# Optimization experiments

Hardware: AMD Instinct MI355X
Metric: run time of the kernel (lower is better)

Reference implementation:

```python
import jax, jax.numpy as jnp
import numpy as np

EPS_BN = 1e-5
EPS_LN = 1e-5
EPS_L2 = 1e-12


def adder2d(x, w, stride):
    """AdderNet pseudo-conv: out = -sum |x_patch - w| (negative L1 distance).
    x: (N, Cin, H, W); w: (Cout, Cin, kh, kw); no padding, no bias.
    Loops only over the small fixed kernel footprint (<=12 positions) to avoid
    materializing the full im2col L1 tensor at once.
    """
    N, Cin, H, W = x.shape
    Cout, _, kh, kw = w.shape
    sh, sw = stride
    Ho = (H - kh) // sh + 1
    Wo = (W - kw) // sw + 1
    out = jnp.zeros((N, Ho, Wo, Cout), dtype=x.dtype)
    for i in range(kh):
        for j in range(kw):
            # strided slice of the input for this kernel tap: (N, Cin, Ho, Wo)
            xs = x[:, :, i:i + sh * Ho:sh, j:j + sw * Wo:sw]
            xs = jnp.transpose(xs, (0, 2, 3, 1))          # (N, Ho, Wo, Cin)
            wt = w[:, :, i, j]                            # (Cout, Cin)
            # |x - w| summed over Cin -> (N, Ho, Wo, Cout)
            out = out - jnp.abs(xs[:, :, :, None, :] - wt[None, None, None, :, :]).sum(-1)
    return jnp.transpose(out, (0, 3, 1, 2))               # (N, Cout, Ho, Wo)


def bn_relu(x, gamma, beta):
    # training-mode BatchNorm2d (batch statistics, biased var) + ReLU
    mean = x.mean(axis=(0, 2, 3), keepdims=True)
    var = x.var(axis=(0, 2, 3), keepdims=True)
    y = (x - mean) * jax.lax.rsqrt(var + EPS_BN)
    y = y * gamma[None, :, None, None] + beta[None, :, None, None]
    return jax.nn.relu(y)


def setup_inputs() -> dict:
    key = jax.random.key(0)
    ks = jax.random.split(key, 8)
    N = 16
    x = jax.random.normal(ks[0], (N, 1, 196, 3), dtype=jnp.float32)
    w1 = jax.random.normal(ks[1], (128, 1, 6, 1), dtype=jnp.float32) * 0.1
    w2 = jax.random.normal(ks[2], (256, 128, 6, 1), dtype=jnp.float32) * 0.05
    w3 = jax.random.normal(ks[3], (384, 256, 6, 2), dtype=jnp.float32) * 0.05
    g1, b1 = jnp.ones((128,), jnp.float32), jnp.zeros((128,), jnp.float32)
    g2, b2 = jnp.ones((256,), jnp.float32), jnp.zeros((256,), jnp.float32)
    g3, b3 = jnp.ones((384,), jnp.float32), jnp.zeros((384,), jnp.float32)
    Wfc = jax.random.normal(ks[4], (6, 16128), dtype=jnp.float32) * (1.0 / np.sqrt(16128))
    bfc = jax.random.normal(ks[5], (6,), dtype=jnp.float32) * 0.01
    return {"x": x, "w1": w1, "g1": g1, "b1": b1, "w2": w2, "g2": g2, "b2": b2,
            "w3": w3, "g3": g3, "b3": b3, "Wfc": Wfc, "bfc": bfc}


def reference(x, w1, g1, b1, w2, g2, b2, w3, g3, b3, Wfc, bfc):
    h = bn_relu(adder2d(x, w1, (2, 1)), g1, b1)   # (N,128,96,3)
    h = bn_relu(adder2d(h, w2, (2, 1)), g2, b2)   # (N,256,46,3)
    h = bn_relu(adder2d(h, w3, (2, 1)), g3, b3)   # (N,384,21,2)
    h = h.reshape(h.shape[0], -1)                  # (N,16128)
    h = h @ Wfc.T + bfc                            # (N,6)
    # nn.LayerNorm(x.size()) normalizes over ALL dims (batch included), weight=1 bias=0
    mu = h.mean()
    var = h.var()
    h = (h - mu) * jax.lax.rsqrt(var + EPS_LN)
    # F.normalize: per-row L2 normalization
    norm = jnp.sqrt((h * h).sum(axis=1, keepdims=True))
    return h / jnp.maximum(norm, EPS_L2)
```

## Files before the change

### kernel.cpp

```cpp
#include <hip/hip_runtime.h>
#include <math.h>

#define DEVINL __device__ __forceinline__

DEVINL float absadd(float a, float b) {
  float t;
  asm("v_add_f32 %0, |%1|, |%2|" : "=v"(t) : "v"(a), "v"(b));
  return t;
}

template<int NWAVES>
DEVINL void block_reduce_2d(double& a, double& b) {
  #pragma unroll
  for (int off = 32; off > 0; off >>= 1) {
    a += __shfl_down(a, off, 64);
    b += __shfl_down(b, off, 64);
  }
  __shared__ double sa[NWAVES], sb[NWAVES];
  const int tid = threadIdx.x;
  const int wid = tid >> 6;
  if ((tid & 63) == 0) { sa[wid] = a; sb[wid] = b; }
  __syncthreads();
  if (tid == 0) {
    double ta = 0.0, tb = 0.0;
    #pragma unroll
    for (int w = 0; w < NWAVES; ++w) { ta += sa[w]; tb += sb[w]; }
    a = ta; b = tb;
  }
}

__global__ __launch_bounds__(256) void k_conv1(
    const float* __restrict__ x, const float* __restrict__ w1,
    const float* __restrict__ g1, const float* __restrict__ b1,
    float* __restrict__ h1) {
  __shared__ float xlds[9408];
  const int co = blockIdx.x;
  const int tid = threadIdx.x;
  {
    float4* xd = (float4*)xlds;
    const float4* xs = (const float4*)x;
    #pragma unroll
    for (int k = 0; k < 10; ++k) {
      const int f = tid + k * 256;
      if (f < 2352) xd[f] = xs[f];
    }
  }
  float wv[6];
  #pragma unroll
  for (int i = 0; i < 6; ++i) wv[i] = w1[co * 6 + i];
  __syncthreads();

  float vals[18];
  double s = 0.0, sq = 0.0;
  #pragma unroll
  for (int k = 0; k < 18; ++k) {
    const int p = tid + k * 256;
    const int n = p / 288;
    const int r = p - n * 288;
    const int ho = r / 3;
    const int wo = r - ho * 3;
    const float* xb = xlds + n * 588 + (2 * ho) * 3 + wo;
    float e0 = xb[0]  - wv[0];
    float e1 = xb[3]  - wv[1];
    float e2 = xb[6]  - wv[2];
    float e3 = xb[9]  - wv[3];
    float e4 = xb[12] - wv[4];
    float e5 = xb[15] - wv[5];
    const float t0 = absadd(e0, e1);
    const float t1 = absadd(e2, e3);
    const float t2 = absadd(e4, e5);
    const float v = -((t0 + t1) + t2);
    vals[k] = v;
    s += (double)v;
    sq += (double)v * (double)v;
  }
  block_reduce_2d<4>(s, sq);
  __shared__ float ssc, ssh;
  if (tid == 0) {
    const double mean = s * (1.0 / 4608.0);
    const double var  = sq * (1.0 / 4608.0) - mean * mean;
    const float rstd = (float)rsqrt(var + 1e-5);
    const float sc = g1[co] * rstd;
    ssc = sc;
    ssh = b1[co] - (float)mean * sc;
  }
  __syncthreads();
  const float sc = ssc, sh = ssh;
  #pragma unroll
  for (int k = 0; k < 18; ++k) {
    const int p = tid + k * 256;
    const int n = p / 288;
    const int r = p - n * 288;
    const int ho = r / 3;
    const int wo = r - ho * 3;
    h1[((n * 128 + co) * 96 + ho) * 3 + wo] = fmaxf(0.f, fmaf(vals[k], sc, sh));
  }
}

__global__ __launch_bounds__(192) void k_conv2p(
    const float* __restrict__ h1, const float* __restrict__ w2,
    float* __restrict__ part2) {
  __shared__ float wlds[512];
  __shared__ float4 xbuf[2][584];
  const int bx = blockIdx.x;
  const int kc = bx & 7;
  const int rbx = bx >> 3;
  const int cg = rbx & 63;
  const int nh = rbx >> 6;
  const int co0 = cg * 4, ci0 = kc * 16, n0 = nh * 8;
  const int tid = threadIdx.x;
  #pragma unroll
  for (int f = tid; f < 512; f += 192) {
    const int cil = f >> 5, rem = f & 31, c = rem >> 3, kk = rem & 7;
    wlds[f] = (kk < 6) ? w2[(co0 + c) * 768 + (ci0 + cil) * 6 + kk] : 0.f;
  }
  const bool active = tid < 184;
  const int n = tid / 23, hp = tid - n * 23;

  int s_lds[3], s_g[3];
  #pragma unroll
  for (int k = 0; k < 3; ++k) {
    const int f = tid + k * 192;
    const int nn = f / 72, j = f - nn * 72;
    s_lds[k] = nn * 73 + j;
    s_g[k]   = (n0 + nn) * 9216 + j;
  }
  const float4* h1v = (const float4*)h1;

  float acc[4][6];
  #pragma unroll
  for (int c = 0; c < 4; ++c)
    #pragma unroll
    for (int o = 0; o < 6; ++o) acc[c][o] = 0.f;

  float4 r[3];
  #pragma unroll
  for (int k = 0; k < 3; ++k) r[k] = h1v[s_g[k] + ci0 * 72];
  #pragma unroll
  for (int k = 0; k < 3; ++k) xbuf[0][s_lds[k]] = r[k];
  #pragma unroll
  for (int k = 0; k < 3; ++k) r[k] = h1v[s_g[k] + (ci0 + 1) * 72];
  __syncthreads();

  const float4* wl4 = (const float4*)wlds;
  #pragma unroll 1
  for (int ci = 0; ci < 16; ++ci) {
    const float4* cur = xbuf[ci & 1];
    if (ci + 1 < 16) {
      float4* nxt = xbuf[(ci + 1) & 1];
      #pragma unroll
      for (int k = 0; k < 3; ++k) nxt[s_lds[k]] = r[k];
    }
    if (ci + 2 < 16) {
      #pragma unroll
      for (int k = 0; k < 3; ++k) r[k] = h1v[s_g[k] + (ci0 + ci + 2) * 72];
    }
    if (active) {
      const float4* xr = cur + n * 73 + hp * 3;
      float xf[24];
      #pragma unroll
      for (int t = 0; t < 6; ++t) {
        const float4 q = xr[t];
        xf[4 * t + 0] = q.x; xf[4 * t + 1] = q.y; xf[4 * t + 2] = q.z; xf[4 * t + 3] = q.w;
      }
      #pragma unroll
      for (int c = 0; c < 4; ++c) {
        const float4 wa = wl4[(ci * 4 + c) * 2];
        const float4 wb = wl4[(ci * 4 + c) * 2 + 1];
        const float wv[6] = {wa.x, wa.y, wa.z, wa.w, wb.x, wb.y};
        #pragma unroll
        for (int po = 0; po < 2; ++po)
          #pragma unroll
          for (int wo = 0; wo < 3; ++wo) {
            float e0 = xf[(2 * po + 0) * 3 + wo] - wv[0];
            float e1 = xf[(2 * po + 1) * 3 + wo] - wv[1];
            float e2 = xf[(2 * po + 2) * 3 + wo] - wv[2];
            float e3 = xf[(2 * po + 3) * 3 + wo] - wv[3];
            float e4 = xf[(2 * po + 4) * 3 + wo] - wv[4];
            float e5 = xf[(2 * po + 5) * 3 + wo] - wv[5];
            const float t0 = absadd(e0, e1);
            const float t1 = absadd(e2, e3);
            const float t2 = absadd(e4, e5);
            acc[c][po * 3 + wo] += (t0 + t1) + t2;
          }
      }
    }
    __syncthreads();
  }
  if (active) {
    #pragma unroll
    for (int c = 0; c < 4; ++c)
      #pragma unroll
      for (int po = 0; po < 2; ++po)
        #pragma unroll
        for (int wo = 0; wo < 3; ++wo) {
          const int p = (n0 + n) * 138 + (2 * hp + po) * 3 + wo;
          part2[(size_t)(kc * 256 + co0 + c) * 2208 + p] = acc[c][po * 3 + wo];
        }
  }
}

__global__ __launch_bounds__(384) void k_combine2(
    const float* __restrict__ part2, const float* __restrict__ g2,
    const float* __restrict__ b2, float* __restrict__ h2) {
  const int co = blockIdx.x;
  const int tid = threadIdx.x;
  const bool active = tid < 368;
  float v[6];
  double s = 0.0, sq = 0.0;
  #pragma unroll
  for (int k = 0; k < 6; ++k) {
    float sum = 0.f;
    if (active) {
      const int p = tid + k * 368;
      #pragma unroll
      for (int kc = 0; kc < 8; ++kc)
        sum += part2[(size_t)(kc * 256 + co) * 2208 + p];
    }
    const float val = -sum;
    v[k] = val;
    if (active) { s += (double)val; sq += (double)val * (double)val; }
  }
  block_reduce_2d<6>(s, sq);
  __shared__ float ssc, ssh;
  if (tid == 0) {
    const double mean = s * (1.0 / 2208.0);
    const double var  = sq * (1.0 / 2208.0) - mean * mean;
    const float rstd = (float)rsqrt(var + 1e-5);
    const float sc = g2[co] * rstd;
    ssc = sc;
    ssh = b2[co] - (float)mean * sc;
  }
  __syncthreads();
  if (active) {
    const float sc = ssc, sh = ssh;
    #pragma unroll
    for (int k = 0; k < 6; ++k) {
      const int p = tid + k * 368;
      const int n = p / 138, rem = p - n * 138;
      h2[n * 35328 + co * 138 + rem] = fmaxf(0.f, fmaf(v[k], sc, sh));
    }
  }
}

__global__ __launch_bounds__(128) void k_conv3p(
    const float* __restrict__ h2, const float* __restrict__ w3,
    float* __restrict__ part3) {
  __shared__ float wlds[768];
  __shared__ float2 xbuf[2][1136];
  const int bx = blockIdx.x;
  const int cg = bx >> 4, kc = bx & 15;
  const int co0 = cg * 4, ci0 = kc * 16;
  const int tid = threadIdx.x;
  #pragma unroll
  for (int f = tid; f < 768; f += 128) {
    const int cil = f / 48, rem = f - cil * 48, c = rem / 12, kk = rem - c * 12;
    wlds[f] = w3[(co0 + c) * 3072 + (ci0 + cil) * 12 + kk];
  }
  const bool active = tid < 112;
  const int n = tid / 7, hot = tid - n * 7;

  int s_lds[9], s_g[9];
  const bool v9 = tid < 80;
  #pragma unroll
  for (int k = 0; k < 9; ++k) {
    const int f = tid + k * 128;
    const int nn = f / 69, j = f - nn * 69;
    s_lds[k] = nn * 71 + j;
    s_g[k]   = nn * 17664 + j;
  }
  const float2* h2v = (const float2*)h2;

  float acc[4][3][2];
  #pragma unroll
  for (int c = 0; c < 4; ++c)
    #pragma unroll
    for (int h = 0; h < 3; ++h) { acc[c][h][0] = 0.f; acc[c][h][1] = 0.f; }

  float2 r[9];
  #pragma unroll
  for (int k = 0; k < 8; ++k) r[k] = h2v[s_g[k] + ci0 * 69];
  if (v9) r[8] = h2v[s_g[8] + ci0 * 69];
  #pragma unroll
  for (int k = 0; k < 8; ++k) xbuf[0][s_lds[k]] = r[k];
  if (v9) xbuf[0][s_lds[8]] = r[8];
  #pragma unroll
  for (int k = 0; k < 8; ++k) r[k] = h2v[s_g[k] + (ci0 + 1) * 69];
  if (v9) r[8] = h2v[s_g[8] + (ci0 + 1) * 69];
  __syncthreads();

  const float4* wl4 = (const float4*)wlds;
  #pragma unroll 1
  for (int ci = 0; ci < 16; ++ci) {
    const float2* cur = xbuf[ci & 1];
    if (ci + 1 < 16) {
      float2* nxt = xbuf[(ci + 1) & 1];
      #pragma unroll
      for (int k = 0; k < 8; ++k) nxt[s_lds[k]] = r[k];
      if (v9) nxt[s_lds[8]] = r[8];
    }
    if (ci + 2 < 16) {
      #pragma unroll
      for (int k = 0; k < 8; ++k) r[k] = h2v[s_g[k] + (ci0 + ci + 2) * 69];
      if (v9) r[8] = h2v[s_g[8] + (ci0 + ci + 2) * 69];
    }
    if (active) {
      float xf[30];
      const float2* xr = cur + n * 71 + 9 * hot;
      #pragma unroll
      for (int t = 0; t < 15; ++t) {
        const float2 q = xr[t];
        xf[2 * t + 0] = q.x; xf[2 * t + 1] = q.y;
      }
      #pragma unroll
      for (int c = 0; c < 4; ++c) {
        const float4 w0 = wl4[(ci * 4 + c) * 3];
        const float4 w1 = wl4[(ci * 4 + c) * 3 + 1];
        const float4 w2q = wl4[(ci * 4 + c) * 3 + 2];
        const float wv[12] = {w0.x, w0.y, w0.z, w0.w, w1.x, w1.y,
                              w1.z, w1.w, w2q.x, w2q.y, w2q.z, w2q.w};
        #pragma unroll
        for (int h = 0; h < 3; ++h)
          #pragma unroll
          for (int wo = 0; wo < 2; ++wo) {
            float e0  = xf[(2 * h + 0) * 3 + wo]     - wv[0];
            float e1  = xf[(2 * h + 0) * 3 + wo + 1] - wv[1];
            float e2  = xf[(2 * h + 1) * 3 + wo]     - wv[2];
            float e3  = xf[(2 * h + 1) * 3 + wo + 1] - wv[3];
            float e4  = xf[(2 * h + 2) * 3 + wo]     - wv[4];
            float e5  = xf[(2 * h + 2) * 3 + wo + 1] - wv[5];
            float e6  = xf[(2 * h + 3) * 3 + wo]     - wv[6];
            float e7  = xf[(2 * h + 3) * 3 + wo + 1] - wv[7];
            float e8  = xf[(2 * h + 4) * 3 + wo]     - wv[8];
            float e9  = xf[(2 * h + 4) * 3 + wo + 1] - wv[9];
            float e10 = xf[(2 * h + 5) * 3 + wo]     - wv[10];
            float e11 = xf[(2 * h + 5) * 3 + wo + 1] - wv[11];
            const float t0 = absadd(e0, e1);
            const float t1 = absadd(e2, e3);
            const float t2 = absadd(e4, e5);
            const float t3 = absadd(e6, e7);
            const float t4 = absadd(e8, e9);
            const float t5 = absadd(e10, e11);
            acc[c][h][wo] += ((t0 + t1) + (t2 + t3)) + (t4 + t5);
          }
      }
    }
    __syncthreads();
  }
  if (active) {
    #pragma unroll
    for (int c = 0; c < 4; ++c)
      #pragma unroll
      for (int h = 0; h < 3; ++h) {
        const int ho = 3 * hot + h;
        #pragma unroll
        for (int wo = 0; wo < 2; ++wo) {
          const int p = n * 42 + ho * 2 + wo;
          part3[(size_t)(kc * 384 + co0 + c) * 672 + p] = acc[c][h][wo];
        }
      }
  }
}

__global__ __launch_bounds__(384) void k_combine3(
    const float* __restrict__ part3, const float* __restrict__ g3,
    const float* __restrict__ b3, float* __restrict__ h3) {
  const int co = blockIdx.x;
  const int tid = threadIdx.x;
  const bool active = tid < 336;
  float v[2];
  double s = 0.0, sq = 0.0;
  #pragma unroll
  for (int k = 0; k < 2; ++k) {
    float sum = 0.f;
    if (active) {
      const int p = tid + k * 336;
      #pragma unroll
      for (int kc = 0; kc < 16; ++kc)
        sum += part3[(size_t)(kc * 384 + co) * 672 + p];
    }
    const float val = -sum;
    v[k] = val;
    if (active) { s += (double)val; sq += (double)val * (double)val; }
  }
  block_reduce_2d<6>(s, sq);
  __shared__ float ssc, ssh;
  if (tid == 0) {
    const double mean = s * (1.0 / 672.0);
    const double var  = sq * (1.0 / 672.0) - mean * mean;
    const float rstd = (float)rsqrt(var + 1e-5);
    const float sc = g3[co] * rstd;
    ssc = sc;
    ssh = b3[co] - (float)mean * sc;
  }
  __syncthreads();
  if (active) {
    const float sc = ssc, sh = ssh;
    #pragma unroll
    for (int k = 0; k < 2; ++k) {
      const int p = tid + k * 336;
      const int n = p / 42, rem = p - n * 42;
      h3[n * 16128 + co * 42 + rem] = fmaxf(0.f, fmaf(v[k], sc, sh));
    }
  }
}

__global__ __launch_bounds__(256) void k_fcp(
    const float* __restrict__ h3, const float* __restrict__ Wfc,
    float* __restrict__ hfcp) {
  const int bx = blockIdx.x;
  const int pair = bx >> 2, q = bx & 3;
  const int n = pair / 6, o = pair - n * 6;
  const float4* xr = (const float4*)(h3 + n * 16128) + q * 1008;
  const float4* wr = (const float4*)(Wfc + o * 16128) + q * 1008;
  float sacc = 0.f;
  for (int k = threadIdx.x; k < 1008; k += 256) {
    const float4 xv = xr[k];
    const float4 wv = wr[k];
    sacc += xv.x * wv.x + xv.y * wv.y + xv.z * wv.z + xv.w * wv.w;
  }
  double d = (double)sacc, dummy = 0.0;
  block_reduce_2d<4>(d, dummy);
  if (threadIdx.x == 0) hfcp[bx] = (float)d;
}

__global__ __launch_bounds__(128) void k_final(
    const float* __restrict__ hfcp, const float* __restrict__ bfc,
    float* __restrict__ out) {
  __shared__ float ys[96];
  __shared__ float params[2];
  const int tid = threadIdx.x;
  float v = 0.f;
  if (tid < 96) {
    v = hfcp[tid * 4 + 0] + hfcp[tid * 4 + 1] + hfcp[tid * 4 + 2] + hfcp[tid * 4 + 3]
        + bfc[tid % 6];
    ys[tid] = v;
  }
  __syncthreads();
  if (tid == 0) {
    double s = 0.0, sq = 0.0;
    for (int i = 0; i < 96; ++i) { const double t = (double)ys[i]; s += t; sq += t * t; }
    const double mu = s / 96.0;
    const double var = sq / 96.0 - mu * mu;
    params[0] = (float)mu;
    params[1] = (float)rsqrt(var + 1e-5);
  }
  __syncthreads();
  const float y = (v - params[0]) * params[1];
  __syncthreads();
  if (tid < 96) ys[tid] = y;
  __syncthreads();
  if (tid < 96) {
    const int n = tid / 6;
    float ss = 0.f;
    #pragma unroll
    for (int k = 0; k < 6; ++k) { const float t = ys[n * 6 + k]; ss += t * t; }
    const float norm = sqrtf(ss);
    out[tid] = y / fmaxf(norm, 1e-12f);
  }
}

extern "C" void kernel_launch(void* const* d_in, const int* in_sizes, int n_in,
                              void* d_out, int out_size, void* d_ws, size_t ws_size,
                              hipStream_t stream) {
  const float* x   = (const float*)d_in[0];
  const float* w1  = (const float*)d_in[1];
  const float* g1  = (const float*)d_in[2];
  const float* b1  = (const float*)d_in[3];
  const float* w2  = (const float*)d_in[4];
  const float* g2  = (const float*)d_in[5];
  const float* b2  = (const float*)d_in[6];
  const float* w3  = (const float*)d_in[7];
  const float* g3  = (const float*)d_in[8];
  const float* b3  = (const float*)d_in[9];
  const float* Wfc = (const float*)d_in[10];
  const float* bfc = (const float*)d_in[11];

  float* ws   = (float*)d_ws;
  float* h1   = ws;
  float* h2   = h1 + 589824;
  float* h3   = h2 + 565248;
  float* hfcp = h3 + 258048;
  float* part = hfcp + 384;
  float* out  = (float*)d_out;

  k_conv1   <<<128, 256, 0, stream>>>(x, w1, g1, b1, h1);
  k_conv2p  <<<1024, 192, 0, stream>>>(h1, w2, part);
  k_combine2<<<256, 384, 0, stream>>>(part, g2, b2, h2);
  k_conv3p  <<<1536, 128, 0, stream>>>(h2, w3, part);
  k_combine3<<<384, 384, 0, stream>>>(part, g3, b3, h3);
  k_fcp     <<<384, 256, 0, stream>>>(h3, Wfc, hfcp);
  k_final   <<<1, 128, 0, stream>>>(hfcp, bfc, out);
}
```

Measured before the change: 132.3 us.

## Remap conv3 work so each lane owns one output channel across all rows

The layer-3 adder kernel is retiled into single-wave blocks of 64 threads. Each block covers 8 output channels and 8 batch items, and each lane owns one channel and one sample, accumulating all 42 outputs in registers. The input row is slid through a register window across the 7 row groups. The double-buffered LDS and __syncthreads are replaced by a single buffer, relying on one-wave lockstep execution. Output is stored as contiguous float2. This removes block barriers and the idle lanes of the old mapping, at the cost of higher register pressure and reliance on implicit intra-wave LDS ordering.

```diff
diff --git a/kernel.cpp b/kernel.cpp
--- a/kernel.cpp
+++ b/kernel.cpp
@@ -243,122 +243,104 @@
   }
 }
 
-__global__ __launch_bounds__(128) void k_conv3p(
+__global__ __launch_bounds__(64) void k_conv3p(
     const float* __restrict__ h2, const float* __restrict__ w3,
     float* __restrict__ part3) {
-  __shared__ float wlds[768];
-  __shared__ float2 xbuf[2][1136];
+  __shared__ float wlds[1536];
+  __shared__ float2 xbuf[560];
   const int bx = blockIdx.x;
-  const int cg = bx >> 4, kc = bx & 15;
-  const int co0 = cg * 4, ci0 = kc * 16;
-  const int tid = threadIdx.x;
-  #pragma unroll
-  for (int f = tid; f < 768; f += 128) {
-    const int cil = f / 48, rem = f - cil * 48, c = rem / 12, kk = rem - c * 12;
+  const int kc = bx & 15;
+  const int rbx = bx >> 4;
+  const int cg = rbx % 48;
+  const int nh = rbx / 48;
+  const int co0 = cg * 8, ci0 = kc * 16, n0 = nh * 8;
+  const int tid = threadIdx.x;
+  #pragma unroll
+  for (int f = tid; f < 1536; f += 64) {
+    const int cil = f / 96, rem = f - cil * 96, c = rem / 12, kk = rem - c * 12;
     wlds[f] = w3[(co0 + c) * 3072 + (ci0 + cil) * 12 + kk];
   }
-  const bool active = tid < 112;
-  const int n = tid / 7, hot = tid - n * 7;
+  const int n = tid >> 3, co = tid & 7;
 
   int s_lds[9], s_g[9];
-  const bool v9 = tid < 80;
+  const bool v9 = tid < 40;
   #pragma unroll
   for (int k = 0; k < 9; ++k) {
-    const int f = tid + k * 128;
+    const int f = tid + k * 64;
     const int nn = f / 69, j = f - nn * 69;
-    s_lds[k] = nn * 71 + j;
-    s_g[k]   = nn * 17664 + j;
+    s_lds[k] = nn * 70 + j;
+    s_g[k]   = (n0 + nn) * 17664 + j;
   }
   const float2* h2v = (const float2*)h2;
 
-  float acc[4][3][2];
-  #pragma unroll
-  for (int c = 0; c < 4; ++c)
-    #pragma unroll
-    for (int h = 0; h < 3; ++h) { acc[c][h][0] = 0.f; acc[c][h][1] = 0.f; }
+  float acc[42];
+  #pragma unroll
+  for (int i = 0; i < 42; ++i) acc[i] = 0.f;
 
   float2 r[9];
   #pragma unroll
   for (int k = 0; k < 8; ++k) r[k] = h2v[s_g[k] + ci0 * 69];
   if (v9) r[8] = h2v[s_g[8] + ci0 * 69];
-  #pragma unroll
-  for (int k = 0; k < 8; ++k) xbuf[0][s_lds[k]] = r[k];
-  if (v9) xbuf[0][s_lds[8]] = r[8];
-  #pragma unroll
-  for (int k = 0; k < 8; ++k) r[k] = h2v[s_g[k] + (ci0 + 1) * 69];
-  if (v9) r[8] = h2v[s_g[8] + (ci0 + 1) * 69];
-  __syncthreads();
-
+
+  const float* xrow = (const float*)xbuf + n * 140;
   const float4* wl4 = (const float4*)wlds;
+
   #pragma unroll 1
   for (int ci = 0; ci < 16; ++ci) {
-    const float2* cur = xbuf[ci & 1];
+    #pragma unroll
+    for (int k = 0; k < 8; ++k) xbuf[s_lds[k]] = r[k];
+    if (v9) xbuf[s_lds[8]] = r[8];
     if (ci + 1 < 16) {
-      float2* nxt = xbuf[(ci + 1) & 1];
-      #pragma unroll
-      for (int k = 0; k < 8; ++k) nxt[s_lds[k]] = r[k];
-      if (v9) nxt[s_lds[8]] = r[8];
-    }
-    if (ci + 2 < 16) {
-      #pragma unroll
-      for (int k = 0; k < 8; ++k) r[k] = h2v[s_g[k] + (ci0 + ci + 2) * 69];
-      if (v9) r[8] = h2v[s_g[8] + (ci0 + ci + 2) * 69];
-    }
-    if (active) {
-      float xf[30];
-      const float2* xr = cur + n * 71 + 9 * hot;
-      #pragma unroll
-      for (int t = 0; t < 15; ++t) {
-        const float2 q = xr[t];
-        xf[2 * t + 0] = q.x; xf[2 * t + 1] = q.y;
-      }
-      #pragma unroll
-      for (int c = 0; c < 4; ++c) {
-        const float4 w0 = wl4[(ci * 4 + c) * 3];
-        const float4 w1 = wl4[(ci * 4 + c) * 3 + 1];
-        const float4 w2q = wl4[(ci * 4 + c) * 3 + 2];
-        const float wv[12] = {w0.x, w0.y, w0.z, w0.w, w1.x, w1.y,
-                              w1.z, w1.w, w2q.x, w2q.y, w2q.z, w2q.w};
-        #pragma unroll
-        for (int h = 0; h < 3; ++h)
-          #pragma unroll
-          for (int wo = 0; wo < 2; ++wo) {
-            float e0  = xf[(2 * h + 0) * 3 + wo]     - wv[0];
-            float e1  = xf[(2 * h + 0) * 3 + wo + 1] - wv[1];
-            float e2  = xf[(2 * h + 1) * 3 + wo]     - wv[2];
-            float e3  = xf[(2 * h + 1) * 3 + wo + 1] - wv[3];
-            float e4  = xf[(2 * h + 2) * 3 + wo]     - wv[4];
-            float e5  = xf[(2 * h + 2) * 3 + wo + 1] - wv[5];
-            float e6  = xf[(2 * h + 3) * 3 + wo]     - wv[6];
-            float e7  = xf[(2 * h + 3) * 3 + wo + 1] - wv[7];
-            float e8  = xf[(2 * h + 4) * 3 + wo]     - wv[8];
-            float e9  = xf[(2 * h + 4) * 3 + wo + 1] - wv[9];
-            float e10 = xf[(2 * h + 5) * 3 + wo]     - wv[10];
-            float e11 = xf[(2 * h + 5) * 3 + wo + 1] - wv[11];
-            const float t0 = absadd(e0, e1);
-            const float t1 = absadd(e2, e3);
-            const float t2 = absadd(e4, e5);
-            const float t3 = absadd(e6, e7);
-            const float t4 = absadd(e8, e9);
-            const float t5 = absadd(e10, e11);
-            acc[c][h][wo] += ((t0 + t1) + (t2 + t3)) + (t4 + t5);
-          }
-      }
-    }
-    __syncthreads();
-  }
-  if (active) {
-    #pragma unroll
-    for (int c = 0; c < 4; ++c)
-      #pragma unroll
-      for (int h = 0; h < 3; ++h) {
-        const int ho = 3 * hot + h;
+      #pragma unroll
+      for (int k = 0; k < 8; ++k) r[k] = h2v[s_g[k] + (ci0 + ci + 1) * 69];
+      if (v9) r[8] = h2v[s_g[8] + (ci0 + ci + 1) * 69];
+    }
+    const float4 w0 = wl4[(ci * 8 + co) * 3];
+    const float4 w1 = wl4[(ci * 8 + co) * 3 + 1];
+    const float4 w2q = wl4[(ci * 8 + co) * 3 + 2];
+    const float wv[12] = {w0.x, w0.y, w0.z, w0.w, w1.x, w1.y,
+                          w1.z, w1.w, w2q.x, w2q.y, w2q.z, w2q.w};
+    float xf[30];
+    #pragma unroll
+    for (int t = 0; t < 30; ++t) xf[t] = xrow[t];
+    #pragma unroll
+    for (int hot = 0; hot < 7; ++hot) {
+      #pragma unroll
+      for (int h = 0; h < 3; ++h)
         #pragma unroll
         for (int wo = 0; wo < 2; ++wo) {
-          const int p = n * 42 + ho * 2 + wo;
-          part3[(size_t)(kc * 384 + co0 + c) * 672 + p] = acc[c][h][wo];
+          float e0  = xf[(2 * h + 0) * 3 + wo]     - wv[0];
+          float e1  = xf[(2 * h + 0) * 3 + wo + 1] - wv[1];
+          float e2  = xf[(2 * h + 1) * 3 + wo]     - wv[2];
+          float e3  = xf[(2 * h + 1) * 3 + wo + 1] - wv[3];
+          float e4  = xf[(2 * h + 2) * 3 + wo]     - wv[4];
+          float e5  = xf[(2 * h + 2) * 3 + wo + 1] - wv[5];
+          float e6  = xf[(2 * h + 3) * 3 + wo]     - wv[6];
+          float e7  = xf[(2 * h + 3) * 3 + wo + 1] - wv[7];
+          float e8  = xf[(2 * h + 4) * 3 + wo]     - wv[8];
+          float e9  = xf[(2 * h + 4) * 3 + wo + 1] - wv[9];
+          float e10 = xf[(2 * h + 5) * 3 + wo]     - wv[10];
+          float e11 = xf[(2 * h + 5) * 3 + wo + 1] - wv[11];
+          const float t0 = absadd(e0, e1);
+          const float t1 = absadd(e2, e3);
+          const float t2 = absadd(e4, e5);
+          const float t3 = absadd(e6, e7);
+          const float t4 = absadd(e8, e9);
+          const float t5 = absadd(e10, e11);
+          acc[(3 * hot + h) * 2 + wo] += ((t0 + t1) + (t2 + t3)) + (t4 + t5);
         }
+      if (hot < 6) {
+        #pragma unroll
+        for (int t = 0; t < 12; ++t) xf[t] = xf[t + 18];
+        #pragma unroll
+        for (int t = 0; t < 18; ++t) xf[12 + t] = xrow[18 * hot + 30 + t];
       }
+    }
+  }
+  {
+    float2* dst = (float2*)(part3 + (size_t)(kc * 384 + co0 + co) * 672 + (n0 + n) * 42);
+    #pragma unroll
+    for (int k = 0; k < 21; ++k) dst[k] = make_float2(acc[2 * k], acc[2 * k + 1]);
   }
 }
 
@@ -487,7 +469,7 @@
   k_conv1   <<<128, 256, 0, stream>>>(x, w1, g1, b1, h1);
   k_conv2p  <<<1024, 192, 0, stream>>>(h1, w2, part);
   k_combine2<<<256, 384, 0, stream>>>(part, g2, b2, h2);
-  k_conv3p  <<<1536, 128, 0, stream>>>(h2, w3, part);
+  k_conv3p  <<<1536, 64, 0, stream>>>(h2, w3, part);
   k_combine3<<<384, 384, 0, stream>>>(part, g3, b3, h3);
   k_fcp     <<<384, 256, 0, stream>>>(h3, Wfc, hfcp);
   k_final   <<<1, 128, 0, stream>>>(hfcp, bfc, out);
```

Result: slower. 135.6 us (+2.5%).
